# Kernel tuning notes

Hardware: AMD Instinct MI355X
Metric: run time of the kernel (lower is better)

Reference implementation:

```python
import jax, jax.numpy as jnp
import numpy as np

DIM = 2048
N_HEADS = 32
N_KV = 8
HEAD_DIM = DIM // N_HEADS  # 64
N_REP = N_HEADS // N_KV    # 4
HALF = HEAD_DIM // 2
B = 2
T = 2048
THETA = 10000.0


def _rope(x, cos, sin):
    # x: [B,H,T,hd]; cos/sin: [T,HALF]. Pairs are interleaved (..., half, 2),
    # matching torch.view_as_complex on a (..., -1, 2) reshape.
    xr = x.reshape(x.shape[:-1] + (HALF, 2))
    x0, x1 = xr[..., 0], xr[..., 1]
    o0 = x0 * cos - x1 * sin
    o1 = x0 * sin + x1 * cos
    return jnp.stack([o0, o1], axis=-1).reshape(x.shape)


def setup_inputs() -> dict:
    key = jax.random.key(0)
    ks = jax.random.split(key, 6)
    x = jax.random.normal(ks[0], (B, T, DIM), dtype=jnp.float32)
    scale = 0.02
    wq = jax.random.normal(ks[1], (N_HEADS * HEAD_DIM, DIM), dtype=jnp.float32) * scale
    wk = jax.random.normal(ks[2], (N_KV * HEAD_DIM, DIM), dtype=jnp.float32) * scale
    wv = jax.random.normal(ks[3], (N_KV * HEAD_DIM, DIM), dtype=jnp.float32) * scale
    wo = jax.random.normal(ks[4], (DIM, DIM), dtype=jnp.float32) * scale
    # causal mask [1,1,T,T]
    mask = jnp.tril(jnp.ones((T, T), dtype=jnp.int32))[None, None]
    # RoPE tables (precompute_freqs_cis with theta=10000, scaling_factor=1.0)
    freqs = 1.0 / THETA ** (jnp.arange(HALF, dtype=jnp.float32) / HALF)
    angles = jnp.arange(2 * T, dtype=jnp.float32)[:, None] * freqs[None, :]
    return {"x": x, "mask": mask, "wq": wq, "wk": wk, "wv": wv, "wo": wo,
            "cos": jnp.cos(angles), "sin": jnp.sin(angles)}


def reference(x, mask, wq, wk, wv, wo, cos, sin):
    Bx, Tx, C = x.shape
    q = (x @ wq.T).reshape(Bx, Tx, N_HEADS, HEAD_DIM).transpose(0, 2, 1, 3)
    k = (x @ wk.T).reshape(Bx, Tx, N_KV, HEAD_DIM).transpose(0, 2, 1, 3)
    v = (x @ wv.T).reshape(Bx, Tx, N_KV, HEAD_DIM).transpose(0, 2, 1, 3)
    q = _rope(q, cos[:Tx], sin[:Tx])
    k = _rope(k, cos[:Tx], sin[:Tx])
    # GQA: head h attends to kv head h // N_REP (repeat_interleave semantics)
    qg = q.reshape(Bx, N_KV, N_REP, Tx, HEAD_DIM)
    att = jnp.einsum('bgrtd,bgsd->bgrts', qg, k) * (HEAD_DIM ** -0.5)
    m = mask[0, 0, :Tx, :Tx]  # broadcast over b,g,r
    att = jnp.where(m == 0, -jnp.inf, att)
    att = jax.nn.softmax(att, axis=-1)
    og = jnp.einsum('bgrts,bgsd->bgrtd', att, v)
    out = og.reshape(Bx, N_HEADS, Tx, HEAD_DIM).transpose(0, 2, 1, 3).reshape(Bx, Tx, C)
    return out @ wo.T
```

## Files before the change

kernel.cpp:

```cpp
#include <hip/hip_runtime.h>
#include <hip/hip_bf16.h>

typedef unsigned short u16;
typedef __attribute__((ext_vector_type(8))) short s16x8;
typedef __attribute__((ext_vector_type(4))) float f32x4;
typedef __attribute__((ext_vector_type(16))) float f32x16;
typedef __attribute__((ext_vector_type(4))) float f32x4v;
typedef __attribute__((ext_vector_type(4))) u16 u16x4;

#define DIM 2048
#define NH 32
#define NKV 8
#define HD 64
#define TT 2048
#define BB 2
#define MT (BB * TT)

__device__ __forceinline__ u16 f2bf(float f) {
    union { float f; unsigned u; } v; v.f = f;
    unsigned r = v.u + 0x7FFFu + ((v.u >> 16) & 1u);
    return (u16)(r >> 16);
}
__device__ __forceinline__ float bf2f(u16 h) {
    union { unsigned u; float f; } v; v.u = ((unsigned)h) << 16;
    return v.f;
}
__device__ __forceinline__ u16 cvtbf(float f) {
    __hip_bfloat16 hb = __float2bfloat16(f);
    return *reinterpret_cast<u16*>(&hb);
}
__device__ __forceinline__ void plane32swap(unsigned& a, unsigned& b) {
#if defined(__has_builtin)
#if __has_builtin(__builtin_amdgcn_permlane32_swap)
    auto t = __builtin_amdgcn_permlane32_swap((int)a, (int)b, false, false);
    a = (unsigned)t[0]; b = (unsigned)t[1];
#else
    asm volatile("v_permlane32_swap_b32 %0, %1" : "+v"(a), "+v"(b));
#endif
#else
    asm volatile("v_permlane32_swap_b32 %0, %1" : "+v"(a), "+v"(b));
#endif
}

__global__ void k_convert_all(const float* __restrict__ x, const float* __restrict__ wq,
                              const float* __restrict__ wk, const float* __restrict__ wv,
                              const float* __restrict__ wo,
                              u16* __restrict__ xb, u16* __restrict__ wqkv, u16* __restrict__ wob) {
    long i = (long)(blockIdx.x * 256 + threadIdx.x) * 4;
    const float* src; u16* dst; long o = i;
    if (o < 8388608L)            { src = x;  dst = xb; }
    else if ((o -= 8388608L) < 4194304L) { src = wq; dst = wqkv; }
    else if ((o -= 4194304L) < 1048576L) { src = wk; dst = wqkv + 4194304L; }
    else if ((o -= 1048576L) < 1048576L) { src = wv; dst = wqkv + 5242880L; }
    else { o -= 1048576L;          src = wo; dst = wob; }
    f32x4v f = *(const f32x4v*)(src + o);
    u16x4 out;
    #pragma unroll
    for (int e = 0; e < 4; ++e) out[e] = f2bf(f[e]);
    *(u16x4*)(dst + o) = out;
}

template<int BNF, bool OUTF32>
__global__ __launch_bounds__(512, 2) void k_gemm256(const u16* __restrict__ A, const u16* __restrict__ B,
                                                    void* __restrict__ C, int M, int N, int K) {
    constexpr int BN = 64 * BNF;
    constexpr int BH = 2048 * BNF;
    __shared__ u16 LDS[32768 + 4 * BH];
    const int nTn = N / BN;
    const int nwg = gridDim.x;
    const int wg = (blockIdx.x & 7) * (nwg >> 3) + (blockIdx.x >> 3);
    const int tm = wg / nTn, tn = wg % nTn;
    const int tid = threadIdx.x, wid = tid >> 6, lane = tid & 63;
    const int wr = wid >> 2, wc = wid & 3;
    const u16* Ab = A + (size_t)tm * 256 * K;
    const u16* Bb = B + (size_t)tn * BN * K;

    f32x4 acc[8][BNF] = {};
    s16x8 af[4], bfr[BNF];

    auto STAGE_A = [&](int buf, int kk, int kt) {
        u16* base = LDS + (buf * 2 + kk) * 8192;
        const u16* g = Ab + kt * 64 + kk * 32;
        #pragma unroll
        for (int i = 0; i < 2; ++i) {
            const int s = i * 512 + tid;
            const int row = s >> 2;
            const int cl = (s & 3) ^ ((row >> 1) & 3);
            __builtin_amdgcn_global_load_lds(
                (const __attribute__((address_space(1))) void*)(g + (size_t)row * K + cl * 8),
                (__attribute__((address_space(3))) void*)(base + (i * 512 + wid * 64) * 8), 16, 0, 0);
        }
    };
    auto STAGE_B = [&](int buf, int kk, int kt) {
        u16* base = LDS + 32768 + (buf * 2 + kk) * BH;
        const u16* g = Bb + kt * 64 + kk * 32;
        auto one = [&](int ch) {
            const int row = ch * 16 + (lane >> 2);
            const int cl = (lane & 3) ^ ((row >> 1) & 3);
            __builtin_amdgcn_global_load_lds(
                (const __attribute__((address_space(1))) void*)(g + (size_t)row * K + cl * 8),
                (__attribute__((address_space(3))) void*)(base + ch * 512), 16, 0, 0);
        };
        if constexpr (BNF == 4) { one(wid); one(8 + wid); }
        else if constexpr (BNF == 3) { one(wid); one(8 + (wid & 3)); }
        else { one(wid); }
    };
    auto LDA = [&](int buf, int kk, int mh) {
        const u16* base = LDS + (buf * 2 + kk) * 8192;
        #pragma unroll
        for (int m2 = 0; m2 < 4; ++m2) {
            const int row = wr * 128 + (mh * 4 + m2) * 16 + (lane & 15);
            const int cl = (lane >> 4) ^ ((row >> 1) & 3);
            af[m2] = *(const s16x8*)(base + row * 32 + cl * 8);
        }
    };
    auto LDB = [&](int buf, int kk) {
        const u16* base = LDS + 32768 + (buf * 2 + kk) * BH;
        #pragma unroll
        for (int n = 0; n < BNF; ++n) {
            const int row = wc * (16 * BNF) + n * 16 + (lane & 15);
            const int cl = (lane >> 4) ^ ((row >> 1) & 3);
            bfr[n] = *(const s16x8*)(base + row * 32 + cl * 8);
        }
    };
    auto MFMA16 = [&](int mh) {
        asm volatile("s_waitcnt lgkmcnt(0)" ::: "memory");
        __builtin_amdgcn_sched_barrier(0);
        __builtin_amdgcn_s_setprio(1);
        #pragma unroll
        for (int m2 = 0; m2 < 4; ++m2)
            #pragma unroll
            for (int n = 0; n < BNF; ++n)
                acc[mh * 4 + m2][n] =
                    __builtin_amdgcn_mfma_f32_16x16x32_bf16(af[m2], bfr[n], acc[mh * 4 + m2][n], 0, 0, 0);
        __builtin_amdgcn_s_setprio(0);
    };

    #define VMID() do { if constexpr (BNF == 2) asm volatile("s_waitcnt vmcnt(6)" ::: "memory"); \
                        else                    asm volatile("s_waitcnt vmcnt(8)" ::: "memory"); } while (0)
    #define VONE() do { if constexpr (BNF == 2) asm volatile("s_waitcnt vmcnt(3)" ::: "memory"); \
                        else                    asm volatile("s_waitcnt vmcnt(4)" ::: "memory"); } while (0)

    STAGE_A(0, 0, 0); STAGE_B(0, 0, 0);
    STAGE_A(0, 1, 0); STAGE_B(0, 1, 0);
    STAGE_A(1, 0, 1); STAGE_B(1, 0, 1);
    VMID();
    __builtin_amdgcn_s_barrier();

    const int NI = K >> 7;
    for (int it = 0; it < NI; ++it) {
        const bool last = (it == NI - 1);
        const int t1 = 2 * it + 1;
        LDA(0, 0, 0); LDB(0, 0);
        STAGE_A(1, 1, t1);
        __builtin_amdgcn_s_barrier();
        MFMA16(0);
        __builtin_amdgcn_s_barrier();

        LDA(0, 0, 1);
        STAGE_B(1, 1, t1);
        __builtin_amdgcn_s_barrier();
        MFMA16(1);
        VMID();
        __builtin_amdgcn_s_barrier();

        LDA(0, 1, 0); LDB(0, 1);
        if (!last) STAGE_A(0, 0, t1 + 1);
        __builtin_amdgcn_s_barrier();
        MFMA16(0);
        __builtin_amdgcn_s_barrier();

        LDA(0, 1, 1);
        if (!last) STAGE_B(0, 0, t1 + 1);
        __builtin_amdgcn_s_barrier();
        MFMA16(1);
        if (!last) VMID(); else VONE();
        __builtin_amdgcn_s_barrier();

        LDA(1, 0, 0); LDB(1, 0);
        if (!last) STAGE_A(0, 1, t1 + 1);
        __builtin_amdgcn_s_barrier();
        MFMA16(0);
        __builtin_amdgcn_s_barrier();

        LDA(1, 0, 1);
        if (!last) STAGE_B(0, 1, t1 + 1);
        __builtin_amdgcn_s_barrier();
        MFMA16(1);
        if (!last) VMID(); else asm volatile("s_waitcnt vmcnt(0)" ::: "memory");
        __builtin_amdgcn_s_barrier();

        LDA(1, 1, 0); LDB(1, 1);
        if (!last) STAGE_A(1, 0, t1 + 2);
        __builtin_amdgcn_s_barrier();
        MFMA16(0);
        __builtin_amdgcn_s_barrier();

        LDA(1, 1, 1);
        if (!last) STAGE_B(1, 0, t1 + 2);
        __builtin_amdgcn_s_barrier();
        MFMA16(1);
        if (!last) VMID();
        __builtin_amdgcn_s_barrier();
    }
    #undef VMID
    #undef VONE

    #pragma unroll
    for (int mf = 0; mf < 8; ++mf)
        #pragma unroll
        for (int n = 0; n < BNF; ++n)
            #pragma unroll
            for (int r = 0; r < 4; ++r) {
                const int row = tm * 256 + wr * 128 + mf * 16 + (lane >> 4) * 4 + r;
                const int col = tn * BN + wc * (16 * BNF) + n * 16 + (lane & 15);
                if (OUTF32) ((float*)C)[(size_t)row * N + col] = acc[mf][n][r];
                else        ((u16*)C)[(size_t)row * N + col] = f2bf(acc[mf][n][r]);
            }
}

__global__ void k_rope(const u16* __restrict__ qkv, const float* __restrict__ ct, const float* __restrict__ st,
                       u16* __restrict__ qo, u16* __restrict__ ko, u16* __restrict__ vo) {
    const int idx = blockIdx.x * 256 + threadIdx.x;
    const int c = idx % 384;
    const int bt = idx / 384;
    const int b = bt / TT, t = bt % TT;
    const s16x8 v = *(const s16x8*)(qkv + (size_t)bt * 3072 + c * 8);
    if (c < 320) {
        const bool isq = c < 256;
        const int base = isq ? c : c - 256;
        const int hh = base >> 3;
        const int di0 = (base & 7) * 4;
        const f32x4v cc = *(const f32x4v*)(ct + t * 32 + di0);
        const f32x4v ss = *(const f32x4v*)(st + t * 32 + di0);
        const float QS = isq ? 0.18033688f : 1.0f;
        s16x8 o;
        #pragma unroll
        for (int p = 0; p < 4; ++p) {
            const float x0 = bf2f((u16)v[2 * p]), x1 = bf2f((u16)v[2 * p + 1]);
            o[2 * p]     = (short)cvtbf((x0 * cc[p] - x1 * ss[p]) * QS);
            o[2 * p + 1] = (short)cvtbf((x0 * ss[p] + x1 * cc[p]) * QS);
        }
        u16* dst = isq ? (qo + ((size_t)(b * NH + hh) * TT + t) * HD + 2 * di0)
                       : (ko + ((size_t)(b * NKV + hh) * TT + t) * HD + 2 * di0);
        *(s16x8*)dst = o;
    } else {
        const int base = c - 320;
        const int hh = base >> 3;
        const int d0 = (base & 7) * 8;
        *(s16x8*)(vo + ((size_t)(b * NKV + hh) * TT + t) * HD + d0) = v;
    }
}

__global__ __launch_bounds__(256) void k_vtrans(const u16* __restrict__ vp, u16* __restrict__ vt) {
    __shared__ u16 tile[64][66];
    const int bg = blockIdx.x >> 5;
    const int t0 = (blockIdx.x & 31) * 64;
    const int tid = threadIdx.x;
    #pragma unroll
    for (int c = 0; c < 2; ++c) {
        const int idx = c * 256 + tid;
        const int tl = idx >> 3, dc = idx & 7;
        s16x8 v = *(const s16x8*)(vp + ((size_t)bg * TT + t0 + tl) * HD + dc * 8);
        *(s16x8*)(&tile[tl][dc * 8]) = v;
    }
    __syncthreads();
    #pragma unroll
    for (int c = 0; c < 2; ++c) {
        const int idx = c * 256 + tid;
        const int d = idx >> 3, tc = idx & 7;
        s16x8 v;
        #pragma unroll
        for (int e = 0; e < 8; ++e) v[e] = (short)tile[tc * 8 + e][d];
        *(s16x8*)(vt + ((size_t)bg * HD + d) * TT + t0 + tc * 8) = v;
    }
}

__global__ __launch_bounds__(256) void k_attn(const u16* __restrict__ Q, const u16* __restrict__ K,
                                              const u16* __restrict__ Vtg, u16* __restrict__ O) {
    const int bid = blockIdx.x;
    const int qt = 15 - (bid >> 6);
    const int bh = bid & 63;
    const int h = bh & 31;
    const int b = bh >> 5;
    const int g = h >> 2;
    __shared__ u16 Ks[3][64 * 64];
    __shared__ u16 Vs[3][64 * 64];
    const int tid = threadIdx.x, wave = tid >> 6, lane = tid & 63;
    const int c = lane & 31, hi = lane >> 5;
    const u16* Qg = Q + ((size_t)(b * NH + h) * TT + qt * 128) * HD;
    const u16* Kg = K + (size_t)(b * NKV + g) * TT * HD;
    const u16* Vg = Vtg + (size_t)(b * NKV + g) * HD * TT;

    s16x8 qa[4];
    #pragma unroll
    for (int kb = 0; kb < 4; ++kb)
        qa[kb] = *(const s16x8*)(Qg + (size_t)(wave * 32 + c) * HD + kb * 16 + hi * 8);

    const int rl = lane >> 3, ccl = lane & 7;
    auto stage = [&](int jj, int bi) {
        u16* Kb = Ks[bi];
        u16* Vb = Vs[bi];
        #pragma unroll
        for (int cc = 0; cc < 2; ++cc) {
            const int r = wave * 16 + cc * 8 + rl;
            const int sc = ccl ^ (r & 7);
            __builtin_amdgcn_global_load_lds(
                (const __attribute__((address_space(1))) void*)(Kg + ((size_t)(jj * 64 + r)) * HD + sc * 8),
                (__attribute__((address_space(3))) void*)(Kb + (wave * 16 + cc * 8) * 64), 16, 0, 0);
            __builtin_amdgcn_global_load_lds(
                (const __attribute__((address_space(1))) void*)(Vg + (size_t)r * TT + jj * 64 + sc * 8),
                (__attribute__((address_space(3))) void*)(Vb + (wave * 16 + cc * 8) * 64), 16, 0, 0);
        }
    };

    f32x16 acc0 = {}, acc1 = {};
    float l = 0.f;
    const int ntiles = 2 * qt + 2;

    stage(0, 0);
    stage(1, 1);

    for (int j = 0; j < ntiles; ++j) {
        if (j < ntiles - 1) asm volatile("s_waitcnt vmcnt(4)" ::: "memory");
        else                asm volatile("s_waitcnt vmcnt(0)" ::: "memory");
        __builtin_amdgcn_s_barrier();
        if (j + 2 < ntiles) stage(j + 2, (j + 2) % 3);
        const int bi = j % 3;
        const u16* Kb = Ks[bi];
        const u16* Vb = Vs[bi];

        f32x16 s0 = {}, s1 = {};
        __builtin_amdgcn_s_setprio(1);
        #pragma unroll
        for (int kb = 0; kb < 4; ++kb) {
            const s16x8 kf0 = *(const s16x8*)(Kb + c * 64 + (((2 * kb + hi) ^ ccl) * 8));
            const s16x8 kf1 = *(const s16x8*)(Kb + (32 + c) * 64 + (((2 * kb + hi) ^ ccl) * 8));
            s0 = __builtin_amdgcn_mfma_f32_32x32x16_bf16(kf0, qa[kb], s0, 0, 0, 0);
            s1 = __builtin_amdgcn_mfma_f32_32x32x16_bf16(kf1, qa[kb], s1, 0, 0, 0);
        }
        __builtin_amdgcn_s_setprio(0);

        if (j >= ntiles - 2) {
            const int q_loc = wave * 32 + c;
            const int kb64 = (j - (ntiles - 2)) * 64;
            #pragma unroll
            for (int r = 0; r < 16; ++r) {
                const int crow = (r & 3) + 8 * (r >> 2) + 4 * hi;
                if (kb64 + crow > q_loc)      s0[r] = -1e30f;
                if (kb64 + 32 + crow > q_loc) s1[r] = -1e30f;
            }
        }
        #pragma unroll
        for (int r = 0; r < 16; ++r) {
            s0[r] = __builtin_amdgcn_exp2f(s0[r]); l += s0[r];
            s1[r] = __builtin_amdgcn_exp2f(s1[r]); l += s1[r];
        }

        unsigned W0[8], W1[8];
        #pragma unroll
        for (int m = 0; m < 8; ++m) {
            float a0f = s0[2 * m], a1f = s0[2 * m + 1];
            float b0f = s1[2 * m], b1f = s1[2 * m + 1];
            asm("v_cvt_pk_bf16_f32 %0, %1, %2" : "=v"(W0[m]) : "v"(a0f), "v"(a1f));
            asm("v_cvt_pk_bf16_f32 %0, %1, %2" : "=v"(W1[m]) : "v"(b0f), "v"(b1f));
        }
        s16x8 pa[4];
        #pragma unroll
        for (int ks = 0; ks < 4; ++ks) {
            const int base = 4 * (ks & 1);
            unsigned a0 = (ks < 2) ? W0[base + 0] : W1[base + 0];
            unsigned b0 = (ks < 2) ? W0[base + 2] : W1[base + 2];
            unsigned a1 = (ks < 2) ? W0[base + 1] : W1[base + 1];
            unsigned b1 = (ks < 2) ? W0[base + 3] : W1[base + 3];
            plane32swap(a0, b0);
            plane32swap(a1, b1);
            union { unsigned w[4]; s16x8 v; } u;
            u.w[0] = a0; u.w[1] = a1; u.w[2] = b0; u.w[3] = b1;
            pa[ks] = u.v;
        }

        __builtin_amdgcn_s_setprio(1);
        #pragma unroll
        for (int kb = 0; kb < 4; ++kb) {
            const s16x8 vb0 = *(const s16x8*)(Vb + c * 64 + (((2 * kb + hi) ^ ccl) * 8));
            const s16x8 vb1 = *(const s16x8*)(Vb + (32 + c) * 64 + (((2 * kb + hi) ^ ccl) * 8));
            acc0 = __builtin_amdgcn_mfma_f32_32x32x16_bf16(pa[kb], vb0, acc0, 0, 0, 0);
            acc1 = __builtin_amdgcn_mfma_f32_32x32x16_bf16(pa[kb], vb1, acc1, 0, 0, 0);
        }
        __builtin_amdgcn_s_setprio(0);
    }

    l += __shfl_xor(l, 32, 64);
    const float inv = 1.0f / l;
    #pragma unroll
    for (int r = 0; r < 16; ++r) {
        const int crow = (r & 3) + 8 * (r >> 2) + 4 * hi;
        const float li = __shfl(inv, crow, 64);
        const size_t row = (size_t)b * TT + qt * 128 + wave * 32 + crow;
        O[row * DIM + h * 64 + c]      = cvtbf(acc0[r] * li);
        O[row * DIM + h * 64 + 32 + c] = cvtbf(acc1[r] * li);
    }
}

extern "C" void kernel_launch(void* const* d_in, const int* in_sizes, int n_in,
                              void* d_out, int out_size, void* d_ws, size_t ws_size,
                              hipStream_t stream) {
    const float* x  = (const float*)d_in[0];
    const float* wq = (const float*)d_in[2];
    const float* wk = (const float*)d_in[3];
    const float* wv = (const float*)d_in[4];
    const float* wo = (const float*)d_in[5];
    const float* ct = (const float*)d_in[6];
    const float* st = (const float*)d_in[7];
    char* ws = (char*)d_ws;
    u16* xb   = (u16*)(ws);
    u16* wqkv = (u16*)(ws + 16777216);
    u16* wob  = (u16*)(ws + 29360128);
    u16* qkv  = (u16*)(ws + 37748736);
    u16* kr   = (u16*)(ws + 62914560);
    u16* vp   = (u16*)(ws + 67108864);
    u16* qr   = xb;
    u16* ao   = qkv;
    u16* vt   = wqkv;

    k_convert_all<<<18432, 256, 0, stream>>>(x, wq, wk, wv, wo, xb, wqkv, wob);

    k_gemm256<3, false><<<(MT / 256) * (3072 / 192), 512, 0, stream>>>(xb, wqkv, qkv, MT, 3072, DIM);
    k_rope<<<MT * 384 / 256, 256, 0, stream>>>(qkv, ct, st, qr, kr, vp);
    k_vtrans<<<BB * NKV * (TT / 64), 256, 0, stream>>>(vp, vt);
    k_attn<<<16 * 64, 256, 0, stream>>>(qr, kr, vt, ao);
    k_gemm256<2, true><<<(MT / 256) * (DIM / 128), 512, 0, stream>>>(ao, wob, d_out, MT, DIM, DIM);
}
```

Measured before the change: 172.2 us.

## Use 256-row query tiles with 8 waves and double-buffered K/V staging

The attention kernel now runs 512-thread blocks that each cover 256 query rows, halving the grid. Each K/V tile loaded into LDS is therefore shared by twice as many query rows. The triple-buffered prefetch is replaced by a double buffer with a full vmcnt(0) wait each iteration, which cuts LDS use but exposes more load latency. Block ordering is changed to interleave long and short causal rows, and per-wave masking is skipped when a tile is entirely visible.

Result: no change. 171.3 us (-0.5%).

```diff
diff --git a/kernel.cpp b/kernel.cpp
--- a/kernel.cpp
+++ b/kernel.cpp
@@ -276,19 +276,20 @@
     }
 }
 
-__global__ __launch_bounds__(256) void k_attn(const u16* __restrict__ Q, const u16* __restrict__ K,
+__global__ __launch_bounds__(512) void k_attn(const u16* __restrict__ Q, const u16* __restrict__ K,
                                               const u16* __restrict__ Vtg, u16* __restrict__ O) {
     const int bid = blockIdx.x;
-    const int qt = 15 - (bid >> 6);
+    const int gq = bid >> 6;
+    const int qt8 = (gq < 4) ? (7 - gq) : (gq - 4);
     const int bh = bid & 63;
     const int h = bh & 31;
     const int b = bh >> 5;
     const int g = h >> 2;
-    __shared__ u16 Ks[3][64 * 64];
-    __shared__ u16 Vs[3][64 * 64];
+    __shared__ u16 Ks[2][4096];
+    __shared__ u16 Vs[2][4096];
     const int tid = threadIdx.x, wave = tid >> 6, lane = tid & 63;
     const int c = lane & 31, hi = lane >> 5;
-    const u16* Qg = Q + ((size_t)(b * NH + h) * TT + qt * 128) * HD;
+    const u16* Qg = Q + ((size_t)(b * NH + h) * TT + qt8 * 256) * HD;
     const u16* Kg = K + (size_t)(b * NKV + g) * TT * HD;
     const u16* Vg = Vtg + (size_t)(b * NKV + g) * HD * TT;
 
@@ -298,37 +299,29 @@
         qa[kb] = *(const s16x8*)(Qg + (size_t)(wave * 32 + c) * HD + kb * 16 + hi * 8);
 
     const int rl = lane >> 3, ccl = lane & 7;
+    const int sc = ccl ^ rl;
     auto stage = [&](int jj, int bi) {
-        u16* Kb = Ks[bi];
-        u16* Vb = Vs[bi];
-        #pragma unroll
-        for (int cc = 0; cc < 2; ++cc) {
-            const int r = wave * 16 + cc * 8 + rl;
-            const int sc = ccl ^ (r & 7);
-            __builtin_amdgcn_global_load_lds(
-                (const __attribute__((address_space(1))) void*)(Kg + ((size_t)(jj * 64 + r)) * HD + sc * 8),
-                (__attribute__((address_space(3))) void*)(Kb + (wave * 16 + cc * 8) * 64), 16, 0, 0);
-            __builtin_amdgcn_global_load_lds(
-                (const __attribute__((address_space(1))) void*)(Vg + (size_t)r * TT + jj * 64 + sc * 8),
-                (__attribute__((address_space(3))) void*)(Vb + (wave * 16 + cc * 8) * 64), 16, 0, 0);
-        }
+        const int r = wave * 8 + rl;
+        __builtin_amdgcn_global_load_lds(
+            (const __attribute__((address_space(1))) void*)(Kg + ((size_t)(jj * 64 + r)) * HD + sc * 8),
+            (__attribute__((address_space(3))) void*)(Ks[bi] + wave * 512), 16, 0, 0);
+        __builtin_amdgcn_global_load_lds(
+            (const __attribute__((address_space(1))) void*)(Vg + (size_t)r * TT + jj * 64 + sc * 8),
+            (__attribute__((address_space(3))) void*)(Vs[bi] + wave * 512), 16, 0, 0);
     };
 
     f32x16 acc0 = {}, acc1 = {};
     float l = 0.f;
-    const int ntiles = 2 * qt + 2;
+    const int ntiles = 4 * qt8 + 4;
 
     stage(0, 0);
-    stage(1, 1);
 
     for (int j = 0; j < ntiles; ++j) {
-        if (j < ntiles - 1) asm volatile("s_waitcnt vmcnt(4)" ::: "memory");
-        else                asm volatile("s_waitcnt vmcnt(0)" ::: "memory");
-        __builtin_amdgcn_s_barrier();
-        if (j + 2 < ntiles) stage(j + 2, (j + 2) % 3);
-        const int bi = j % 3;
-        const u16* Kb = Ks[bi];
-        const u16* Vb = Vs[bi];
+        asm volatile("s_waitcnt vmcnt(0)" ::: "memory");
+        __builtin_amdgcn_s_barrier();
+        if (j + 1 < ntiles) stage(j + 1, (j + 1) & 1);
+        const u16* Kb = Ks[j & 1];
+        const u16* Vb = Vs[j & 1];
 
         f32x16 s0 = {}, s1 = {};
         __builtin_amdgcn_s_setprio(1);
@@ -341,14 +334,16 @@
         }
         __builtin_amdgcn_s_setprio(0);
 
-        if (j >= ntiles - 2) {
-            const int q_loc = wave * 32 + c;
-            const int kb64 = (j - (ntiles - 2)) * 64;
-            #pragma unroll
-            for (int r = 0; r < 16; ++r) {
-                const int crow = (r & 3) + 8 * (r >> 2) + 4 * hi;
-                if (kb64 + crow > q_loc)      s0[r] = -1e30f;
-                if (kb64 + 32 + crow > q_loc) s1[r] = -1e30f;
+        if (j >= ntiles - 4) {
+            const int kb64 = (j - (ntiles - 4)) * 64;
+            if (kb64 + 63 > wave * 32) {
+                const int q_loc = wave * 32 + c;
+                #pragma unroll
+                for (int r = 0; r < 16; ++r) {
+                    const int crow = (r & 3) + 8 * (r >> 2) + 4 * hi;
+                    if (kb64 + crow > q_loc)      s0[r] = -1e30f;
+                    if (kb64 + 32 + crow > q_loc) s1[r] = -1e30f;
+                }
             }
         }
         #pragma unroll
@@ -397,7 +392,7 @@
     for (int r = 0; r < 16; ++r) {
         const int crow = (r & 3) + 8 * (r >> 2) + 4 * hi;
         const float li = __shfl(inv, crow, 64);
-        const size_t row = (size_t)b * TT + qt * 128 + wave * 32 + crow;
+        const size_t row = (size_t)b * TT + qt8 * 256 + wave * 32 + crow;
         O[row * DIM + h * 64 + c]      = cvtbf(acc0[r] * li);
         O[row * DIM + h * 64 + 32 + c] = cvtbf(acc1[r] * li);
     }
@@ -429,6 +424,6 @@
     k_gemm256<3, false><<<(MT / 256) * (3072 / 192), 512, 0, stream>>>(xb, wqkv, qkv, MT, 3072, DIM);
     k_rope<<<MT * 384 / 256, 256, 0, stream>>>(qkv, ct, st, qr, kr, vp);
     k_vtrans<<<BB * NKV * (TT / 64), 256, 0, stream>>>(vp, vt);
-    k_attn<<<16 * 64, 256, 0, stream>>>(qr, kr, vt, ao);
+    k_attn<<<8 * 64, 512, 0, stream>>>(qr, kr, vt, ao);
     k_gemm256<2, true><<<(MT / 256) * (DIM / 128), 512, 0, stream>>>(ao, wob, d_out, MT, DIM, DIM);
 }
```
